# Kernel optimization log

Hardware: AMD Instinct MI355X
Metric: run time of the kernel (lower is better)

## Reference

```python
import jax, jax.numpy as jnp
import numpy as np

B, T, D, H = 4, 1024, 1024, 16


def setup_inputs() -> dict:
    key = jax.random.key(0)
    ks = jax.random.split(key, 7)
    x = jax.random.normal(ks[0], (B, T, D), dtype=jnp.float32)
    scale = 0.02
    Wq = jax.random.normal(ks[1], (D, D), dtype=jnp.float32) * scale
    Wk = jax.random.normal(ks[2], (D, D), dtype=jnp.float32) * scale
    Wv = jax.random.normal(ks[3], (D, D), dtype=jnp.float32) * scale
    bq = jax.random.normal(ks[4], (D,), dtype=jnp.float32) * scale
    bk = jax.random.normal(ks[5], (D,), dtype=jnp.float32) * scale
    bv = jax.random.normal(ks[6], (D,), dtype=jnp.float32) * scale
    temperature = jnp.ones((H, 1, 1), dtype=jnp.float32)  # nn.Parameter(torch.ones(H,1,1))
    return {"x": x, "Wq": Wq, "bq": bq, "Wk": Wk, "bk": bk, "Wv": Wv, "bv": bv,
            "temperature": temperature}


def reference(x, Wq, bq, Wk, bk, Wv, bv, temperature):
    b, t, d = x.shape
    h = temperature.shape[0]
    dh = d // h
    # torch: self.q(x).view(B, H, -1, T)  -- a RAW reshape of (B,T,D) -> (B,H,Dh,T)
    q = (x @ Wq + bq).reshape(b, h, dh, t)
    k = (x @ Wk + bk).reshape(b, h, dh, t)
    v = (x @ Wv + bv).reshape(b, h, dh, t)
    # attn = k^T @ v : (B,H,T,T), scaled per-head by temperature, softmax over last dim
    attn = jnp.einsum('bhdt,bhds->bhts', k, v) * temperature
    attn = jax.nn.softmax(attn, axis=-1)
    # out = q @ attn : (B,H,Dh,T), then RAW reshape back to (B,T,D)
    out = jnp.einsum('bhdt,bhts->bhds', q, attn)
    return out.reshape(b, t, d)
```

## Files before the change

### kernel.cpp

```cpp
#include <hip/hip_runtime.h>
#include <math.h>

#define Bv 4
#define Tv 1024
#define Dv 1024
#define Hv 16
#define DHv 64
#define L2E 1.4426950408889634f

typedef __attribute__((ext_vector_type(8))) short short8;
typedef __attribute__((ext_vector_type(4))) short short4v;
typedef __attribute__((ext_vector_type(4))) float f32x4;
typedef __attribute__((ext_vector_type(2))) int int2v;

#define MFMA16(a, b, c) __builtin_amdgcn_mfma_f32_16x16x32_bf16((a), (b), (c), 0, 0, 0)

__device__ __forceinline__ short f2bf(float f) {
    union { float f; unsigned u; } v; v.f = f;
    unsigned r = v.u + 0x7FFFu + ((v.u >> 16) & 1u);
    return (short)(r >> 16);
}

__device__ __forceinline__ float exp2_hw(float x) {
#if __has_builtin(__builtin_amdgcn_exp2f)
    return __builtin_amdgcn_exp2f(x);
#else
    return exp2f(x);
#endif
}
__device__ __forceinline__ float log2_hw(float x) {
#if __has_builtin(__builtin_amdgcn_logf)
    return __builtin_amdgcn_logf(x);
#else
    return log2f(x);
#endif
}

__device__ __forceinline__ int cvt_pk_bf16(float lo, float hi) {
    int r; asm("v_cvt_pk_bf16_f32 %0, %1, %2" : "=v"(r) : "v"(lo), "v"(hi)); return r;
}

__device__ __forceinline__ void async16(const void* g, void* l) {
    __builtin_amdgcn_global_load_lds(
        (const __attribute__((address_space(1))) void*)g,
        (__attribute__((address_space(3))) void*)l, 16, 0, 0);
}

__device__ __forceinline__ short8 frag64(const short* buf, int r, int cw) {
    return *(const short8*)&buf[r * 64 + ((cw ^ (r & 7)) << 3)];
}

__device__ __forceinline__ short8 frag32(const short* buf, int r, int cw) {
    return *(const short8*)&buf[r * 32 + (((cw ^ (r >> 1)) & 3) << 3)];
}

__device__ __forceinline__ void lds_barrier() {
    asm volatile("s_waitcnt lgkmcnt(0)" ::: "memory");
    __builtin_amdgcn_sched_barrier(0);
    __builtin_amdgcn_s_barrier();
    __builtin_amdgcn_sched_barrier(0);
}

__global__ __launch_bounds__(256) void cast_x(const float* __restrict__ x, short* __restrict__ xb) {
    const int idx = blockIdx.x * 256 + threadIdx.x;
    float4 v = ((const float4*)x)[idx];
    short4v o;
    o[0] = f2bf(v.x); o[1] = f2bf(v.y); o[2] = f2bf(v.z); o[3] = f2bf(v.w);
    ((short4v*)xb)[idx] = o;
}

__global__ __launch_bounds__(256) void w_cast_t(
    const float* __restrict__ Wq, const float* __restrict__ Wk, const float* __restrict__ Wv,
    short* __restrict__ Wt)
{
    const float* W = (blockIdx.z == 0) ? Wq : (blockIdx.z == 1) ? Wk : Wv;
    short* Wto = Wt + (size_t)blockIdx.z * 1048576;
    __shared__ short Tl[64 * 72];
    const int k0 = blockIdx.y * 64, n0 = blockIdx.x * 64;
    const int tid = threadIdx.x;
    {
        const int r = tid >> 2, c16 = (tid & 3) * 16;
        const float* src = W + (size_t)(k0 + r) * Dv + n0 + c16;
        float4 f0 = ((const float4*)src)[0], f1 = ((const float4*)src)[1];
        float4 f2 = ((const float4*)src)[2], f3 = ((const float4*)src)[3];
        short8 s0, s1;
        s0[0] = f2bf(f0.x); s0[1] = f2bf(f0.y); s0[2] = f2bf(f0.z); s0[3] = f2bf(f0.w);
        s0[4] = f2bf(f1.x); s0[5] = f2bf(f1.y); s0[6] = f2bf(f1.z); s0[7] = f2bf(f1.w);
        s1[0] = f2bf(f2.x); s1[1] = f2bf(f2.y); s1[2] = f2bf(f2.z); s1[3] = f2bf(f2.w);
        s1[4] = f2bf(f3.x); s1[5] = f2bf(f3.y); s1[6] = f2bf(f3.z); s1[7] = f2bf(f3.w);
        *(short8*)&Tl[r * 72 + c16] = s0;
        *(short8*)&Tl[r * 72 + c16 + 8] = s1;
    }
    __syncthreads();
#pragma unroll
    for (int p = 0; p < 2; p++) {
        const int n = p * 32 + (tid >> 3), j8 = (tid & 7) * 8;
        short8 o;
#pragma unroll
        for (int jj = 0; jj < 8; jj++) o[jj] = Tl[(j8 + jj) * 72 + n];
        *(short8*)&Wto[(size_t)(n0 + n) * Dv + k0 + j8] = o;
    }
}

__device__ __forceinline__ void stage_tile(
    const short* __restrict__ xb, const short* __restrict__ Wt,
    const int* aOff, const int* bOff, const int* dOff,
    short* smem, int sl, int k)
{
#pragma unroll
    for (int p = 0; p < 2; p++) {
        async16(xb + aOff[p] + k, smem + sl + dOff[p]);
        async16(Wt + bOff[p] + k, smem + 24576 + sl + dOff[p]);
    }
}

__device__ __forceinline__ void compute_tile(
    const short* smem, int sl, int RM, int CN, int c, int q, f32x4 acc[8][4])
{
    const short* Ac = smem + sl;
    const short* Bc = smem + 24576 + sl;
    short8 bf[4], af[8];
#pragma unroll
    for (int j = 0; j < 4; j++) bf[j] = frag32(Bc, CN + j * 16 + c, q);
#pragma unroll
    for (int m = 0; m < 8; m++) af[m] = frag32(Ac, RM + m * 16 + c, q);
    __builtin_amdgcn_s_setprio(1);
#pragma unroll
    for (int m = 0; m < 8; m++)
#pragma unroll
        for (int j = 0; j < 4; j++)
            acc[m][j] = MFMA16(af[m], bf[j], acc[m][j]);
    __builtin_amdgcn_s_setprio(0);
}

__global__ __launch_bounds__(512, 2) void qkv_mfma(
    const short* __restrict__ xb, const short* __restrict__ Wt3,
    const float* __restrict__ bq, const float* __restrict__ bk, const float* __restrict__ bv,
    const float* __restrict__ temp,
    short* __restrict__ Qo, short* __restrict__ Kt, short* __restrict__ Vt)
{
    const int z = blockIdx.z;
    const short* Wt = Wt3 + (size_t)z * 1048576;
    const float* bias = (z == 0) ? bq : (z == 1) ? bk : bv;

    __shared__ short smem[49152];

    const int tid = threadIdx.x;
    const int lane = tid & 63, w = tid >> 6;
    const int q = lane >> 4, c = lane & 15;
    const int wr = w >> 2, wc = w & 3;
    const int RM = wr * 128, CN = wc * 64;
    const int bm = blockIdx.y * 256, bn = blockIdx.x * 256;

    int aOff[2], bOff[2], dOff[2];
#pragma unroll
    for (int p = 0; p < 2; p++) {
        const int idx = p * 512 + tid;
        const int r = idx >> 2, cs = idx & 3, cg = (cs ^ (r >> 1)) & 3;
        aOff[p] = (bm + r) * Dv + cg * 8;
        bOff[p] = (bn + r) * Dv + cg * 8;
        dOff[p] = idx * 8;
    }

    f32x4 acc[8][4] = {};

    stage_tile(xb, Wt, aOff, bOff, dOff, smem, 0, 0);
    stage_tile(xb, Wt, aOff, bOff, dOff, smem, 8192, 32);

    int slC = 0, slS = 16384;
#pragma unroll 1
    for (int i = 0; i < 30; i++) {
        asm volatile("s_waitcnt vmcnt(4)" ::: "memory");
        __builtin_amdgcn_s_barrier();
        __builtin_amdgcn_sched_barrier(0);
        stage_tile(xb, Wt, aOff, bOff, dOff, smem, slS, (i + 2) * 32);
        compute_tile(smem, slC, RM, CN, c, q, acc);
        slC += 8192; if (slC == 24576) slC = 0;
        slS += 8192; if (slS == 24576) slS = 0;
    }
    asm volatile("s_waitcnt vmcnt(4)" ::: "memory");
    __builtin_amdgcn_s_barrier();
    __builtin_amdgcn_sched_barrier(0);
    compute_tile(smem, slC, RM, CN, c, q, acc);
    slC += 8192; if (slC == 24576) slC = 0;
    asm volatile("s_waitcnt vmcnt(0)" ::: "memory");
    __builtin_amdgcn_s_barrier();
    __builtin_amdgcn_sched_barrier(0);
    compute_tile(smem, slC, RM, CN, c, q, acc);

    if (z == 0) {
#pragma unroll
        for (int j = 0; j < 4; j++) {
            const int col = bn + CN + j * 16 + c;
            const float bb = bias[col];
#pragma unroll
            for (int m = 0; m < 8; m++) {
#pragma unroll
                for (int r = 0; r < 4; r++) {
                    const int row = bm + RM + m * 16 + q * 4 + r;
                    Qo[(size_t)row * Dv + col] = f2bf(acc[m][j][r] + bb);
                }
            }
        }
    } else {
        float scl[2] = {1.f, 1.f};
        if (z == 1) {
            const int h0 = ((bm + RM) >> 6) & 15;
            scl[0] = temp[h0] * L2E;
            scl[1] = temp[(h0 + 1) & 15] * L2E;
        }
        short* dst = (z == 1) ? Kt : Vt;
        short* T = smem;
        const int hb = bm >> 6;
#pragma unroll
        for (int nh = 0; nh < 2; nh++) {
            __syncthreads();
            if ((wc >> 1) == nh) {
#pragma unroll
                for (int j = 0; j < 4; j++) {
                    const int nl = (wc & 1) * 64 + j * 16 + c;
                    const float bb = bias[bn + nh * 128 + nl];
#pragma unroll
                    for (int m = 0; m < 8; m++) {
                        const float s = scl[m >> 2];
                        int2v pk;
                        pk[0] = cvt_pk_bf16((acc[m][j][0] + bb) * s, (acc[m][j][1] + bb) * s);
                        pk[1] = cvt_pk_bf16((acc[m][j][2] + bb) * s, (acc[m][j][3] + bb) * s);
                        *(int2v*)&T[nl * 264 + RM + m * 16 + q * 4] = pk;
                    }
                }
            }
            __syncthreads();
#pragma unroll
            for (int p = 0; p < 8; p++) {
                const int idx = p * 512 + tid;
                const int n = idx >> 5, k2 = idx & 31;
                short8 v = *(const short8*)&T[n * 264 + k2 * 8];
                const size_t addr = (size_t)(hb + (k2 >> 3)) * 65536 +
                                    (size_t)(bn + nh * 128 + n) * 64 + (k2 & 7) * 8;
                *(short8*)&dst[addr] = v;
            }
        }
    }
}

__global__ __launch_bounds__(256, 4) void attn_stats(
    const short* __restrict__ Kt, const short* __restrict__ Vt,
    float* __restrict__ mzOut)
{
    const int L = blockIdx.x + 16 * (blockIdx.y + 16 * blockIdx.z);
    const int bh = (L & 7) + 8 * (L >> 7);
    const int t0 = ((L >> 3) & 15) * 64;
    __shared__ short Ks[64 * 64];
    __shared__ short Vs[2][128 * 64];
    const int tid = threadIdx.x;
    const int lane = tid & 63, w = tid >> 6;
    const int q = lane >> 4, c = lane & 15;
    const short* Kbase = Kt + (size_t)bh * 65536;
    const short* Vbase = Vt + (size_t)bh * 65536;

    int vOff[4], vDst[4];
#pragma unroll
    for (int p = 0; p < 4; p++) {
        const int idx = p * 256 + tid;
        const int r = idx >> 3, cs = idx & 7, cg = cs ^ (r & 7);
        vOff[p] = r * 64 + cg * 8;
        vDst[p] = idx * 8;
    }
#pragma unroll
    for (int p = 0; p < 2; p++) {
        const int idx = p * 256 + tid;
        const int r = idx >> 3, cs = idx & 7, cg = cs ^ (r & 7);
        async16(Kbase + (size_t)(t0 + r) * 64 + cg * 8, Ks + idx * 8);
    }
#pragma unroll
    for (int p = 0; p < 4; p++) async16(Vbase + vOff[p], &Vs[0][0] + vDst[p]);

    float z_run[4] = {0.f, 0.f, 0.f, 0.f};

    short8 aK0, aK1;
#pragma unroll 1
    for (int i = 0; i < 8; i++) {
        __syncthreads();
        if (i < 7) {
            const short* src = Vbase + (i + 1) * 8192;
#pragma unroll
            for (int p = 0; p < 4; p++) async16(src + vOff[p], &Vs[(i + 1) & 1][0] + vDst[p]);
        }
        if (i == 0) {
            aK0 = frag64(Ks, w * 16 + c, q);
            aK1 = frag64(Ks, w * 16 + c, 4 + q);
        }
        const short* Vc = &Vs[i & 1][0];
        __builtin_amdgcn_s_setprio(1);
#pragma unroll
        for (int sf = 0; sf < 8; sf++) {
            short8 b0 = frag64(Vc, sf * 16 + c, q);
            short8 b1 = frag64(Vc, sf * 16 + c, 4 + q);
            f32x4 l = {0.f, 0.f, 0.f, 0.f};
            l = MFMA16(aK0, b0, l);
            l = MFMA16(aK1, b1, l);
#pragma unroll
            for (int r = 0; r < 4; r++) z_run[r] += exp2_hw(l[r]);
        }
        __builtin_amdgcn_s_setprio(0);
    }
#pragma unroll
    for (int mask = 1; mask <= 8; mask <<= 1) {
#pragma unroll
        for (int r = 0; r < 4; r++) z_run[r] += __shfl_xor(z_run[r], mask, 64);
    }
    if (c == 0) {
#pragma unroll
        for (int r = 0; r < 4; r++) {
            const int t = t0 + w * 16 + q * 4 + r;
            mzOut[(size_t)bh * Tv + t] = log2_hw(z_run[r]);
        }
    }
}

__global__ __launch_bounds__(256, 2) void attn_out(
    const short* __restrict__ Qb, const short* __restrict__ Kt, const short* __restrict__ Vt,
    const float* __restrict__ mzIn, float* __restrict__ out)
{
    const int L = blockIdx.x + 8 * (blockIdx.y + 16 * blockIdx.z);
    const int bh = (L & 7) + 8 * (L >> 6);
    const int s0 = ((L >> 3) & 7) * 128;
    const int b = bh >> 4, h = bh & 15;

    __shared__ short smem[26624];
    short* VsPt = smem;
    float* mzs = (float*)(smem + 24576);

    const int tid = threadIdx.x;
    const int lane = tid & 63, w = tid >> 6;
    const int q = lane >> 4, c = lane & 15;
    const short* Vbase = Vt + (size_t)bh * 65536;
    const short* Kbase = Kt + (size_t)bh * 65536;
    const short* Qbase = Qb + (size_t)(b * Tv + h * DHv) * Dv;

    int kOff[2], qOff[2], dK[2], dQ[2];
#pragma unroll
    for (int p = 0; p < 2; p++) {
        const int idx = p * 256 + tid;
        const int r = idx >> 3, cs = idx & 7, cg = cs ^ (r & 7);
        kOff[p] = r * 64 + cg * 8;
        qOff[p] = r * 1024 + cg * 8;
        dK[p] = idx * 8;
        dQ[p] = 4096 + idx * 8;
    }

#pragma unroll
    for (int p = 0; p < 4; p++) {
        const int idx = p * 256 + tid;
        const int r = idx >> 3, cs = idx & 7, cg = cs ^ (r & 7);
        async16(Vbase + (size_t)(s0 + r) * 64 + cg * 8, VsPt + idx * 8);
    }
    async16(mzIn + (size_t)bh * Tv + tid * 4, (short*)mzs + tid * 8);
#pragma unroll
    for (int p = 0; p < 2; p++) {
        async16(Kbase + kOff[p], smem + 8192 + dK[p]);
        async16(Qbase + qOff[p], smem + 8192 + dQ[p]);
    }
    __syncthreads();

    short8 vb0[8], vb1[8];
#pragma unroll
    for (int sf = 0; sf < 8; sf++) {
        vb0[sf] = frag64(VsPt, sf * 16 + c, q);
        vb1[sf] = frag64(VsPt, sf * 16 + c, 4 + q);
    }

    f32x4 acc[8] = {};
    short* Pt = VsPt;

#pragma unroll 1
    for (int i = 0; i < 16; i++) {
        const short* kq = smem + 8192 + (i & 1) * 8192;
        __syncthreads();
        if (i < 15) {
            short* nxt = smem + 8192 + ((i + 1) & 1) * 8192;
            const int t1 = (i + 1) * 64;
#pragma unroll
            for (int p = 0; p < 2; p++) {
                async16(Kbase + t1 * 64 + kOff[p], nxt + dK[p]);
                async16(Qbase + t1 + qOff[p], nxt + dQ[p]);
            }
        }
        short8 aK0 = frag64(kq, w * 16 + c, q);
        short8 aK1 = frag64(kq, w * 16 + c, 4 + q);
        const int tr0 = i * 64 + w * 16 + q * 4;
        const float4 mv = *(const float4*)&mzs[tr0];
#pragma unroll
        for (int sf = 0; sf < 8; sf++) {
            f32x4 l = {0.f, 0.f, 0.f, 0.f};
            l = MFMA16(aK0, vb0[sf], l);
            l = MFMA16(aK1, vb1[sf], l);
            const int rr = sf * 16 + c;
            int2v p4;
            p4[0] = cvt_pk_bf16(exp2_hw(l[0] - mv.x), exp2_hw(l[1] - mv.y));
            p4[1] = cvt_pk_bf16(exp2_hw(l[2] - mv.z), exp2_hw(l[3] - mv.w));
            *(int2v*)&Pt[rr * 64 + (((w * 2 + (q >> 1)) ^ (rr & 7)) << 3) + (q & 1) * 4] = p4;
        }
        lds_barrier();
        const short* Qs = kq + 4096;
        short8 aQ0 = frag64(Qs, w * 16 + c, q);
        short8 aQ1 = frag64(Qs, w * 16 + c, 4 + q);
        __builtin_amdgcn_s_setprio(1);
#pragma unroll
        for (int sf = 0; sf < 8; sf++) {
            short8 p0 = frag64(Pt, sf * 16 + c, q);
            short8 p1 = frag64(Pt, sf * 16 + c, 4 + q);
            acc[sf] = MFMA16(aQ0, p0, acc[sf]);
            acc[sf] = MFMA16(aQ1, p1, acc[sf]);
        }
        __builtin_amdgcn_s_setprio(0);
    }

#pragma unroll
    for (int sf = 0; sf < 8; sf++) {
#pragma unroll
        for (int r = 0; r < 4; r++) {
            const int d = w * 16 + q * 4 + r;
            out[(size_t)(b * Tv + h * DHv + d) * Dv + s0 + sf * 16 + c] = acc[sf][r];
        }
    }
}

extern "C" void kernel_launch(void* const* d_in, const int* in_sizes, int n_in,
                              void* d_out, int out_size, void* d_ws, size_t ws_size,
                              hipStream_t stream) {
    const float* x    = (const float*)d_in[0];
    const float* Wq   = (const float*)d_in[1];
    const float* bq   = (const float*)d_in[2];
    const float* Wk   = (const float*)d_in[3];
    const float* bk   = (const float*)d_in[4];
    const float* Wv   = (const float*)d_in[5];
    const float* bv   = (const float*)d_in[6];
    const float* temp = (const float*)d_in[7];
    float* out = (float*)d_out;

    char* ws = (char*)d_ws;
    short* xb = (short*)(ws);
    short* Wt = (short*)(ws + ((size_t)8 << 20));
    short* Qb = (short*)(ws + ((size_t)14 << 20));
    short* Kt = (short*)(ws + ((size_t)22 << 20));
    short* Vt = (short*)(ws + ((size_t)30 << 20));
    float* mzbuf = (float*)(ws + ((size_t)38 << 20));

    cast_x<<<4096, 256, 0, stream>>>(x, xb);
    w_cast_t<<<dim3(16, 16, 3), 256, 0, stream>>>(Wq, Wk, Wv, Wt);
    qkv_mfma<<<dim3(4, 16, 3), 512, 0, stream>>>(xb, Wt, bq, bk, bv, temp, Qb, Kt, Vt);
    attn_stats<<<dim3(16, 16, 4), 256, 0, stream>>>(Kt, Vt, mzbuf);
    attn_out<<<dim3(8, 16, 4), 256, 0, stream>>>(Qb, Kt, Vt, mzbuf, out);
}
```

Baseline: 160.7 us.

## Fuse Q/K/V projections into one GEMM sharing x tiles with k-blocked packed layout

The QKV projection kernel now computes all three outputs in each block: one x tile (128 rows) is loaded per k-step and multiplied against three weight tiles, instead of running three separate GEMMs over z. x and the transposed weights are written in a k-block-major packed layout (32-wide k slices laid out contiguously), so each async load reads a contiguous panel. The block tile shrinks from 256x256 per matrix to 128x128 per matrix. The grid grows to 256 blocks, and the epilogue is reworked for the smaller tile. This reuses A-tile loads across Q, K and V and improves load contiguity. The cost is 96 accumulators per thread and more LDS traffic for B relative to A.

```diff
diff --git a/kernel.cpp b/kernel.cpp
--- a/kernel.cpp
+++ b/kernel.cpp
@@ -54,19 +54,15 @@
     return *(const short8*)&buf[r * 32 + (((cw ^ (r >> 1)) & 3) << 3)];
 }
 
-__device__ __forceinline__ void lds_barrier() {
-    asm volatile("s_waitcnt lgkmcnt(0)" ::: "memory");
-    __builtin_amdgcn_sched_barrier(0);
-    __builtin_amdgcn_s_barrier();
-    __builtin_amdgcn_sched_barrier(0);
-}
-
-__global__ __launch_bounds__(256) void cast_x(const float* __restrict__ x, short* __restrict__ xb) {
+__global__ __launch_bounds__(256) void cast_x(const float* __restrict__ x, short* __restrict__ xp) {
     const int idx = blockIdx.x * 256 + threadIdx.x;
-    float4 v = ((const float4*)x)[idx];
-    short4v o;
-    o[0] = f2bf(v.x); o[1] = f2bf(v.y); o[2] = f2bf(v.z); o[3] = f2bf(v.w);
-    ((short4v*)xb)[idx] = o;
+    const int t = idx >> 7, j = idx & 127;
+    const float* src = x + (size_t)t * 1024 + j * 8;
+    float4 f0 = ((const float4*)src)[0], f1 = ((const float4*)src)[1];
+    short8 o;
+    o[0] = f2bf(f0.x); o[1] = f2bf(f0.y); o[2] = f2bf(f0.z); o[3] = f2bf(f0.w);
+    o[4] = f2bf(f1.x); o[5] = f2bf(f1.y); o[6] = f2bf(f1.z); o[7] = f2bf(f1.w);
+    *(short8*)&xp[(j >> 2) * 131072 + t * 32 + (j & 3) * 8] = o;
 }
 
 __global__ __launch_bounds__(256) void w_cast_t(
@@ -98,148 +94,124 @@
         short8 o;
 #pragma unroll
         for (int jj = 0; jj < 8; jj++) o[jj] = Tl[(j8 + jj) * 72 + n];
-        *(short8*)&Wto[(size_t)(n0 + n) * Dv + k0 + j8] = o;
-    }
-}
-
-__device__ __forceinline__ void stage_tile(
-    const short* __restrict__ xb, const short* __restrict__ Wt,
-    const int* aOff, const int* bOff, const int* dOff,
-    short* smem, int sl, int k)
-{
-#pragma unroll
-    for (int p = 0; p < 2; p++) {
-        async16(xb + aOff[p] + k, smem + sl + dOff[p]);
-        async16(Wt + bOff[p] + k, smem + 24576 + sl + dOff[p]);
-    }
-}
-
-__device__ __forceinline__ void compute_tile(
-    const short* smem, int sl, int RM, int CN, int c, int q, f32x4 acc[8][4])
-{
-    const short* Ac = smem + sl;
-    const short* Bc = smem + 24576 + sl;
-    short8 bf[4], af[8];
-#pragma unroll
-    for (int j = 0; j < 4; j++) bf[j] = frag32(Bc, CN + j * 16 + c, q);
-#pragma unroll
-    for (int m = 0; m < 8; m++) af[m] = frag32(Ac, RM + m * 16 + c, q);
-    __builtin_amdgcn_s_setprio(1);
-#pragma unroll
-    for (int m = 0; m < 8; m++)
-#pragma unroll
-        for (int j = 0; j < 4; j++)
-            acc[m][j] = MFMA16(af[m], bf[j], acc[m][j]);
-    __builtin_amdgcn_s_setprio(0);
+        const int kk = k0 + j8;
+        *(short8*)&Wto[(kk >> 5) * 32768 + (size_t)(n0 + n) * 32 + (kk & 31)] = o;
+    }
 }
 
 __global__ __launch_bounds__(512, 2) void qkv_mfma(
-    const short* __restrict__ xb, const short* __restrict__ Wt3,
+    const short* __restrict__ xp, const short* __restrict__ Wp,
     const float* __restrict__ bq, const float* __restrict__ bk, const float* __restrict__ bv,
     const float* __restrict__ temp,
     short* __restrict__ Qo, short* __restrict__ Kt, short* __restrict__ Vt)
 {
-    const int z = blockIdx.z;
-    const short* Wt = Wt3 + (size_t)z * 1048576;
-    const float* bias = (z == 0) ? bq : (z == 1) ? bk : bv;
-
     __shared__ short smem[49152];
 
     const int tid = threadIdx.x;
     const int lane = tid & 63, w = tid >> 6;
     const int q = lane >> 4, c = lane & 15;
     const int wr = w >> 2, wc = w & 3;
-    const int RM = wr * 128, CN = wc * 64;
-    const int bm = blockIdx.y * 256, bn = blockIdx.x * 256;
-
-    int aOff[2], bOff[2], dOff[2];
-#pragma unroll
-    for (int p = 0; p < 2; p++) {
-        const int idx = p * 512 + tid;
-        const int r = idx >> 2, cs = idx & 3, cg = (cs ^ (r >> 1)) & 3;
-        aOff[p] = (bm + r) * Dv + cg * 8;
-        bOff[p] = (bn + r) * Dv + cg * 8;
-        dOff[p] = idx * 8;
-    }
-
-    f32x4 acc[8][4] = {};
-
-    stage_tile(xb, Wt, aOff, bOff, dOff, smem, 0, 0);
-    stage_tile(xb, Wt, aOff, bOff, dOff, smem, 8192, 32);
-
-    int slC = 0, slS = 16384;
+    const int n0 = blockIdx.x * 128, tm0 = blockIdx.y * 128;
+
+    const int sr = tid >> 2, scs = tid & 3, scg = (scs ^ (sr >> 1)) & 3;
+    const int aOff = (tm0 + sr) * 32 + scg * 8;
+    const int bOff = (n0 + sr) * 32 + scg * 8;
+    const int dOff = tid * 8;
+
+    f32x4 acc[3][4][2] = {};
+
+    auto stage = [&](int s, int kb) {
+        async16(xp + kb * 131072 + aOff, smem + s * 4096 + dOff);
+#pragma unroll
+        for (int z = 0; z < 3; z++)
+            async16(Wp + z * 1048576 + kb * 32768 + bOff,
+                    smem + 12288 + (s * 3 + z) * 4096 + dOff);
+    };
+    auto compute = [&](int s) {
+        const short* Ac = smem + s * 4096;
+        short8 af[4];
+#pragma unroll
+        for (int m = 0; m < 4; m++) af[m] = frag32(Ac, wr * 64 + m * 16 + c, q);
+        __builtin_amdgcn_s_setprio(1);
+#pragma unroll
+        for (int z = 0; z < 3; z++) {
+            const short* Bc = smem + 12288 + (s * 3 + z) * 4096;
+            short8 b0 = frag32(Bc, wc * 32 + c, q);
+            short8 b1 = frag32(Bc, wc * 32 + 16 + c, q);
+#pragma unroll
+            for (int m = 0; m < 4; m++) {
+                acc[z][m][0] = MFMA16(af[m], b0, acc[z][m][0]);
+                acc[z][m][1] = MFMA16(af[m], b1, acc[z][m][1]);
+            }
+        }
+        __builtin_amdgcn_s_setprio(0);
+    };
+
+    stage(0, 0); stage(1, 1);
+
+    int sC = 0, sS = 2;
 #pragma unroll 1
     for (int i = 0; i < 30; i++) {
         asm volatile("s_waitcnt vmcnt(4)" ::: "memory");
         __builtin_amdgcn_s_barrier();
         __builtin_amdgcn_sched_barrier(0);
-        stage_tile(xb, Wt, aOff, bOff, dOff, smem, slS, (i + 2) * 32);
-        compute_tile(smem, slC, RM, CN, c, q, acc);
-        slC += 8192; if (slC == 24576) slC = 0;
-        slS += 8192; if (slS == 24576) slS = 0;
+        stage(sS, i + 2);
+        compute(sC);
+        sC = (sC == 2) ? 0 : sC + 1;
+        sS = (sS == 2) ? 0 : sS + 1;
     }
     asm volatile("s_waitcnt vmcnt(4)" ::: "memory");
     __builtin_amdgcn_s_barrier();
     __builtin_amdgcn_sched_barrier(0);
-    compute_tile(smem, slC, RM, CN, c, q, acc);
-    slC += 8192; if (slC == 24576) slC = 0;
+    compute(sC);
+    sC = (sC == 2) ? 0 : sC + 1;
     asm volatile("s_waitcnt vmcnt(0)" ::: "memory");
     __builtin_amdgcn_s_barrier();
     __builtin_amdgcn_sched_barrier(0);
-    compute_tile(smem, slC, RM, CN, c, q, acc);
-
-    if (z == 0) {
-#pragma unroll
-        for (int j = 0; j < 4; j++) {
-            const int col = bn + CN + j * 16 + c;
-            const float bb = bias[col];
-#pragma unroll
-            for (int m = 0; m < 8; m++) {
-#pragma unroll
-                for (int r = 0; r < 4; r++) {
-                    const int row = bm + RM + m * 16 + q * 4 + r;
-                    Qo[(size_t)row * Dv + col] = f2bf(acc[m][j][r] + bb);
-                }
+    compute(sC);
+
+#pragma unroll
+    for (int jj = 0; jj < 2; jj++) {
+        const int col = n0 + wc * 32 + jj * 16 + c;
+        const float bb = bq[col];
+#pragma unroll
+        for (int m = 0; m < 4; m++)
+#pragma unroll
+            for (int rr = 0; rr < 4; rr++) {
+                const int row = tm0 + wr * 64 + m * 16 + q * 4 + rr;
+                Qo[(size_t)row * Dv + col] = f2bf(acc[0][m][jj][rr] + bb);
             }
-        }
-    } else {
-        float scl[2] = {1.f, 1.f};
-        if (z == 1) {
-            const int h0 = ((bm + RM) >> 6) & 15;
-            scl[0] = temp[h0] * L2E;
-            scl[1] = temp[(h0 + 1) & 15] * L2E;
-        }
+    }
+    const int hb = tm0 >> 6;
+#pragma unroll
+    for (int z = 1; z < 3; z++) {
+        const float* bias = (z == 1) ? bk : bv;
         short* dst = (z == 1) ? Kt : Vt;
+        float scl = 1.f;
+        if (z == 1) scl = temp[(hb + wr) & 15] * L2E;
+        __syncthreads();
         short* T = smem;
-        const int hb = bm >> 6;
-#pragma unroll
-        for (int nh = 0; nh < 2; nh++) {
-            __syncthreads();
-            if ((wc >> 1) == nh) {
-#pragma unroll
-                for (int j = 0; j < 4; j++) {
-                    const int nl = (wc & 1) * 64 + j * 16 + c;
-                    const float bb = bias[bn + nh * 128 + nl];
-#pragma unroll
-                    for (int m = 0; m < 8; m++) {
-                        const float s = scl[m >> 2];
-                        int2v pk;
-                        pk[0] = cvt_pk_bf16((acc[m][j][0] + bb) * s, (acc[m][j][1] + bb) * s);
-                        pk[1] = cvt_pk_bf16((acc[m][j][2] + bb) * s, (acc[m][j][3] + bb) * s);
-                        *(int2v*)&T[nl * 264 + RM + m * 16 + q * 4] = pk;
-                    }
-                }
+#pragma unroll
+        for (int jj = 0; jj < 2; jj++) {
+            const int nl = wc * 32 + jj * 16 + c;
+            const float bb = bias[n0 + nl];
+#pragma unroll
+            for (int m = 0; m < 4; m++) {
+                int2v pk;
+                pk[0] = cvt_pk_bf16((acc[z][m][jj][0] + bb) * scl, (acc[z][m][jj][1] + bb) * scl);
+                pk[1] = cvt_pk_bf16((acc[z][m][jj][2] + bb) * scl, (acc[z][m][jj][3] + bb) * scl);
+                *(int2v*)&T[nl * 136 + wr * 64 + m * 16 + q * 4] = pk;
             }
-            __syncthreads();
-#pragma unroll
-            for (int p = 0; p < 8; p++) {
-                const int idx = p * 512 + tid;
-                const int n = idx >> 5, k2 = idx & 31;
-                short8 v = *(const short8*)&T[n * 264 + k2 * 8];
-                const size_t addr = (size_t)(hb + (k2 >> 3)) * 65536 +
-                                    (size_t)(bn + nh * 128 + n) * 64 + (k2 & 7) * 8;
-                *(short8*)&dst[addr] = v;
-            }
+        }
+        __syncthreads();
+#pragma unroll
+        for (int p = 0; p < 4; p++) {
+            const int idx = p * 512 + tid;
+            const int n = idx >> 4, k2 = idx & 15;
+            short8 v = *(const short8*)&T[n * 136 + k2 * 8];
+            const size_t addr = (size_t)(hb + (k2 >> 3)) * 65536 +
+                                (size_t)(n0 + n) * 64 + (k2 & 7) * 8;
+            *(short8*)&dst[addr] = v;
         }
     }
 }
@@ -402,7 +374,10 @@
             p4[1] = cvt_pk_bf16(exp2_hw(l[2] - mv.z), exp2_hw(l[3] - mv.w));
             *(int2v*)&Pt[rr * 64 + (((w * 2 + (q >> 1)) ^ (rr & 7)) << 3) + (q & 1) * 4] = p4;
         }
-        lds_barrier();
+        asm volatile("s_waitcnt lgkmcnt(0)" ::: "memory");
+        __builtin_amdgcn_sched_barrier(0);
+        __builtin_amdgcn_s_barrier();
+        __builtin_amdgcn_sched_barrier(0);
         const short* Qs = kq + 4096;
         short8 aQ0 = frag64(Qs, w * 16 + c, q);
         short8 aQ1 = frag64(Qs, w * 16 + c, 4 + q);
@@ -441,16 +416,16 @@
     float* out = (float*)d_out;
 
     char* ws = (char*)d_ws;
-    short* xb = (short*)(ws);
-    short* Wt = (short*)(ws + ((size_t)8 << 20));
+    short* xp = (short*)(ws);
+    short* Wp = (short*)(ws + ((size_t)8 << 20));
     short* Qb = (short*)(ws + ((size_t)14 << 20));
     short* Kt = (short*)(ws + ((size_t)22 << 20));
     short* Vt = (short*)(ws + ((size_t)30 << 20));
     float* mzbuf = (float*)(ws + ((size_t)38 << 20));
 
-    cast_x<<<4096, 256, 0, stream>>>(x, xb);
-    w_cast_t<<<dim3(16, 16, 3), 256, 0, stream>>>(Wq, Wk, Wv, Wt);
-    qkv_mfma<<<dim3(4, 16, 3), 512, 0, stream>>>(xb, Wt, bq, bk, bv, temp, Qb, Kt, Vt);
+    cast_x<<<2048, 256, 0, stream>>>(x, xp);
+    w_cast_t<<<dim3(16, 16, 3), 256, 0, stream>>>(Wq, Wk, Wv, Wp);
+    qkv_mfma<<<dim3(8, 32), 512, 0, stream>>>(xp, Wp, bq, bk, bv, temp, Qb, Kt, Vt);
     attn_stats<<<dim3(16, 16, 4), 256, 0, stream>>>(Kt, Vt, mzbuf);
     attn_out<<<dim3(8, 16, 4), 256, 0, stream>>>(Qb, Kt, Vt, mzbuf, out);
 }
```

Measured after the change: 154.1 us. 4.1% less time.
